# Optimization experiments

Hardware: AMD Instinct MI355X
Metric: run time of the kernel (lower is better)

Reference implementation:

```python
import jax, jax.numpy as jnp
import numpy as np

N = 2_000_000   # active voxels
CIN = 16
COUT = 32
K2 = 9          # 3x3 kernel offsets


def setup_inputs() -> dict:
    key = jax.random.key(0)
    ks = jax.random.split(key, 6)
    x = jax.random.normal(ks[0], (N, CIN), dtype=jnp.float32)
    # per-offset neighbor map: nbr_idx[k, i] = input voxel feeding output i at offset k
    nbr_idx = jax.random.randint(ks[1], (K2, N), 0, N, dtype=jnp.int32)
    nbr_mask = jax.random.uniform(ks[2], (K2, N)) < 0.85
    # center offset is always the voxel itself and always valid
    nbr_idx = nbr_idx.at[K2 // 2].set(jnp.arange(N, dtype=jnp.int32))
    nbr_mask = nbr_mask.at[K2 // 2].set(True)
    s1 = 1.0 / np.sqrt(K2 * CIN)
    s2 = 1.0 / np.sqrt(K2 * COUT)
    sp = 1.0 / np.sqrt(CIN)
    W1 = jax.random.uniform(ks[3], (K2, CIN, COUT), jnp.float32, -s1, s1)
    b1 = jnp.zeros((COUT,), jnp.float32)
    W2 = jax.random.uniform(ks[4], (K2, COUT, COUT), jnp.float32, -s2, s2)
    b2 = jnp.zeros((COUT,), jnp.float32)
    Wp = jax.random.uniform(ks[5], (CIN, COUT), jnp.float32, -sp, sp)
    bp = jnp.zeros((COUT,), jnp.float32)
    return {"x": x, "W1": W1, "b1": b1, "W2": W2, "b2": b2,
            "Wp": Wp, "bp": bp, "nbr_idx": nbr_idx, "nbr_mask": nbr_mask}


def _sparse_conv(feats, W, b, nbr_idx, nbr_mask):
    """Gather-GEMM-accumulate sparse conv.
    feats: [N, Cin]; W: [K2, Cin, Cout]; nbr_idx/nbr_mask: [K2, N].
    Scans over the K2 kernel offsets so only one [N, Cin] gather lives at a time.
    """
    acc0 = jnp.zeros((feats.shape[0], W.shape[-1]), feats.dtype)

    def step(acc, kin):
        idx, m, Wk = kin
        g = feats[idx] * m[:, None].astype(feats.dtype)  # masked gather [N, Cin]
        return acc + g @ Wk, None

    acc, _ = jax.lax.scan(step, acc0, (nbr_idx, nbr_mask, W))
    return acc + b


def reference(x, W1, b1, W2, b2, Wp, bp, nbr_idx, nbr_mask):
    h = jax.nn.relu(_sparse_conv(x, W1, b1, nbr_idx, nbr_mask))
    h = _sparse_conv(h, W2, b2, nbr_idx, nbr_mask)
    identity = x @ Wp + bp  # 1x1 sparse projection (in_ch != out_ch)
    return jax.nn.relu(h + identity)
```

## Files before the change

### kernel.cpp

```cpp
#include <hip/hip_runtime.h>
#include <stdint.h>

#define CIN  16
#define COUT 32
#define K2   9

typedef __attribute__((ext_vector_type(8)))  short bf16x8;
typedef __attribute__((ext_vector_type(16))) float f32x16;
typedef __attribute__((ext_vector_type(4)))  float f32x4;

__device__ __forceinline__ uint16_t f2bf(float f) {
    union { float f; uint32_t u; } a; a.f = f;
    uint32_t u = a.u;
    uint32_t r = u + 0x7FFFu + ((u >> 16) & 1u);
    return (uint16_t)(r >> 16);
}
__device__ __forceinline__ float bf2f(uint32_t b16) {
    union { uint32_t u; float f; } a; a.u = b16 << 16; return a.f;
}

__global__ void detect_mask_kernel(const uint32_t* __restrict__ mw,
                                   int* __restrict__ flag,
                                   float* __restrict__ zrow, int n) {
    int t = threadIdx.x;
    uint32_t w = mw[(size_t)4 * (size_t)n + (size_t)t];
    unsigned long long b = __ballot(w == 1u);
    if (t == 0) *flag = (b == ~0ull) ? 1 : 0;
    if (t < 16) zrow[t] = 0.0f;
}

__global__ void __launch_bounds__(256, 4)
conv1_kernel(const float* __restrict__ x,
             const float* __restrict__ W1,
             const float* __restrict__ b1,
             const int*   __restrict__ nidx,
             const void*  __restrict__ nmask,
             const int*   __restrict__ mflag,
             const char*  __restrict__ zrow,
             uint16_t*    __restrict__ hbuf,
             int n)
{
    __shared__ __align__(16) uint16_t smw[K2 * 2 * 32 * 8];

    for (int i = threadIdx.x; i < K2 * 2 * 32 * 8; i += 256) {
        const int e = i & 7, c2 = (i >> 3) & 31, hf = (i >> 8) & 1, k = i >> 9;
        smw[i] = f2bf(W1[k * (CIN * COUT) + (hf * 8 + e) * COUT + c2]);
    }
    __syncthreads();

    const int lane = threadIdx.x & 63;
    const int wid  = threadIdx.x >> 6;
    const int col  = lane & 31;
    const int half = lane >> 5;
    const int mode32 = *mflag;
    const int*     m32 = (const int*)nmask;
    const uint8_t* m8  = (const uint8_t*)nmask;

    const float bias = b1[col];
    const int ntiles = (n + 31) >> 5;

    for (int tile = blockIdx.x * 4 + wid; tile < ntiles; tile += gridDim.x * 4) {
        const int vbase = tile << 5;
        const int vr = vbase + col;
        const int vc = (vr < n) ? vr : (n - 1);

        int idv[K2];
        uint32_t mb = 0;
        #pragma unroll
        for (int k = 0; k < K2; ++k) {
            const size_t e = (size_t)k * (size_t)n + (size_t)vc;
            idv[k] = __builtin_nontemporal_load(nidx + e);
            const int m = mode32 ? (__builtin_nontemporal_load(m32 + e) != 0)
                                 : (__builtin_nontemporal_load(m8  + e) != 0);
            mb |= (uint32_t)m << k;
        }

        f32x4 ga[K2], gb[K2];
        #pragma unroll
        for (int k = 0; k < K2; ++k) {
            const float* p = ((mb >> k) & 1u)
                ? (x + (size_t)(uint32_t)idv[k] * CIN + half * 8)
                : (const float*)(zrow + half * 32);
            ga[k] = ((const f32x4*)p)[0];
            gb[k] = ((const f32x4*)p)[1];
        }

        f32x16 acc = {};
        #pragma unroll
        for (int k = 0; k < K2; ++k) {
            const bf16x8 Bf = *(const bf16x8*)&smw[((k * 2 + half) * 32 + col) * 8];
            bf16x8 hi, lo;
            #pragma unroll
            for (int e = 0; e < 8; ++e) {
                const float xv = (e < 4) ? ga[k][e] : gb[k][e - 4];
                const uint16_t hb = f2bf(xv);
                hi[e] = (short)hb;
                lo[e] = (short)f2bf(xv - bf2f(hb));
            }
            acc = __builtin_amdgcn_mfma_f32_32x32x16_bf16(hi, Bf, acc, 0, 0, 0);
            acc = __builtin_amdgcn_mfma_f32_32x32x16_bf16(lo, Bf, acc, 0, 0, 0);
        }

        #pragma unroll
        for (int r = 0; r < 16; ++r) {
            const int row = (r & 3) + 8 * (r >> 2) + 4 * half;
            const int vo = vbase + row;
            if (vo < n) {
                const float o = fmaxf(acc[r] + bias, 0.0f);
                hbuf[(size_t)vo * COUT + col] = f2bf(o);
            }
        }
    }
}

__global__ void __launch_bounds__(256, 4)
conv2_kernel(const float* __restrict__ x,
             const float* __restrict__ W2,
             const float* __restrict__ b2,
             const float* __restrict__ Wp,
             const float* __restrict__ bp,
             const int*   __restrict__ nidx,
             const void*  __restrict__ nmask,
             const int*   __restrict__ mflag,
             const char*  __restrict__ zrow,
             const uint16_t* __restrict__ hbuf,
             float*       __restrict__ out,
             int n)
{
    __shared__ __align__(16) uint16_t smw[K2 * 4 * 32 * 8 + 2 * 32 * 8];

    for (int i = threadIdx.x; i < K2 * 4 * 32 * 8 + 2 * 32 * 8; i += 256) {
        uint16_t v;
        if (i < K2 * 4 * 32 * 8) {
            const int e = i & 7, c2 = (i >> 3) & 31, hf = (i >> 8) & 1,
                      cb = (i >> 9) & 1, k = i >> 10;
            v = f2bf(W2[k * (COUT * COUT) + (cb * 16 + hf * 8 + e) * COUT + c2]);
        } else {
            const int j = i - K2 * 4 * 32 * 8;
            const int e = j & 7, c2 = (j >> 3) & 31, hf = (j >> 8) & 1;
            v = f2bf(Wp[(hf * 8 + e) * COUT + c2]);
        }
        smw[i] = v;
    }
    __syncthreads();

    const int lane = threadIdx.x & 63;
    const int wid  = threadIdx.x >> 6;
    const int col  = lane & 31;
    const int half = lane >> 5;
    const int mode32 = *mflag;
    const int*     m32 = (const int*)nmask;
    const uint8_t* m8  = (const uint8_t*)nmask;

    const float bias = b2[col] + bp[col];
    const int ntiles = (n + 31) >> 5;

    for (int tile = blockIdx.x * 4 + wid; tile < ntiles; tile += gridDim.x * 4) {
        const int vbase = tile << 5;
        const int vr = vbase + col;
        const int vc = (vr < n) ? vr : (n - 1);

        int idv[K2];
        uint32_t mb = 0;
        #pragma unroll
        for (int k = 0; k < K2; ++k) {
            const size_t e = (size_t)k * (size_t)n + (size_t)vc;
            idv[k] = __builtin_nontemporal_load(nidx + e);
            const int m = mode32 ? (__builtin_nontemporal_load(m32 + e) != 0)
                                 : (__builtin_nontemporal_load(m8  + e) != 0);
            mb |= (uint32_t)m << k;
        }

        const f32x4* xr = (const f32x4*)(x + (size_t)vc * CIN + half * 8);
        const f32x4 xa = __builtin_nontemporal_load(xr);
        const f32x4 xb = __builtin_nontemporal_load(xr + 1);

        bf16x8 A0[K2], A1[K2];
        #pragma unroll
        for (int k = 0; k < K2; ++k) {
            const char* p = ((mb >> k) & 1u)
                ? (const char*)hbuf + (size_t)(uint32_t)idv[k] * (COUT * 2)
                : zrow;
            A0[k] = *(const bf16x8*)(p + half * 16);
            A1[k] = *(const bf16x8*)(p + 32 + half * 16);
        }

        f32x16 acc = {};

        {
            bf16x8 hi, lo;
            #pragma unroll
            for (int e = 0; e < 8; ++e) {
                const float xv = (e < 4) ? xa[e] : xb[e - 4];
                const uint16_t hb = f2bf(xv);
                hi[e] = (short)hb;
                lo[e] = (short)f2bf(xv - bf2f(hb));
            }
            const bf16x8 Bp = *(const bf16x8*)&smw[K2 * 4 * 32 * 8 + (half * 32 + col) * 8];
            acc = __builtin_amdgcn_mfma_f32_32x32x16_bf16(hi, Bp, acc, 0, 0, 0);
            acc = __builtin_amdgcn_mfma_f32_32x32x16_bf16(lo, Bp, acc, 0, 0, 0);
        }

        #pragma unroll
        for (int k = 0; k < K2; ++k) {
            const bf16x8 B0 = *(const bf16x8*)&smw[(((k * 2 + 0) * 2 + half) * 32 + col) * 8];
            const bf16x8 B1 = *(const bf16x8*)&smw[(((k * 2 + 1) * 2 + half) * 32 + col) * 8];
            acc = __builtin_amdgcn_mfma_f32_32x32x16_bf16(A0[k], B0, acc, 0, 0, 0);
            acc = __builtin_amdgcn_mfma_f32_32x32x16_bf16(A1[k], B1, acc, 0, 0, 0);
        }

        #pragma unroll
        for (int r = 0; r < 16; ++r) {
            const int row = (r & 3) + 8 * (r >> 2) + 4 * half;
            const int vo = vbase + row;
            if (vo < n) {
                const float o = fmaxf(acc[r] + bias, 0.0f);
                __builtin_nontemporal_store(o, out + (size_t)vo * COUT + col);
            }
        }
    }
}

extern "C" void kernel_launch(void* const* d_in, const int* in_sizes, int n_in,
                              void* d_out, int out_size, void* d_ws, size_t ws_size,
                              hipStream_t stream) {
    const float* x    = (const float*)d_in[0];
    const float* W1   = (const float*)d_in[1];
    const float* b1   = (const float*)d_in[2];
    const float* W2   = (const float*)d_in[3];
    const float* b2   = (const float*)d_in[4];
    const float* Wp   = (const float*)d_in[5];
    const float* bp   = (const float*)d_in[6];
    const int*   nidx = (const int*)d_in[7];
    const void*  nmask = d_in[8];
    const int n = in_sizes[0] / CIN;

    int*      mflag = (int*)d_ws;
    float*    zrowf = (float*)((char*)d_ws + 64);
    uint16_t* hbuf  = (uint16_t*)((char*)d_ws + 256);

    detect_mask_kernel<<<1, 64, 0, stream>>>((const uint32_t*)nmask, mflag, zrowf, n);

    const int ntiles = (n + 31) / 32;
    int grid = (ntiles + 3) / 4;
    if (grid > 2048) grid = 2048;

    conv1_kernel<<<grid, 256, 0, stream>>>(x, W1, b1, nidx, nmask, mflag,
                                           (const char*)zrowf, hbuf, n);
    conv2_kernel<<<grid, 256, 0, stream>>>(x, W2, b2, Wp, bp, nidx, nmask, mflag,
                                           (const char*)zrowf, hbuf, (float*)d_out, n);
}
```

Before: 1.007 ms.

## Prefetch next tile's neighbor indices and gather unconditionally, masking after load

Both conv kernels now load the next tile's neighbor indices while the current tile is being processed, taking the index load off the gather's dependency chain. Gathers are always issued from the neighbor index, so they no longer wait on the mask load. The mask is applied after the gather by zeroing the values, which removes the zero-row workspace buffer. Launch bounds change to waves_per_eu(3,4), which allows more registers per thread for the prefetched state. The cost is extra gather traffic for masked neighbors and higher register pressure.

```diff
diff --git a/kernel.cpp b/kernel.cpp
--- a/kernel.cpp
+++ b/kernel.cpp
@@ -20,23 +20,21 @@
 }
 
 __global__ void detect_mask_kernel(const uint32_t* __restrict__ mw,
-                                   int* __restrict__ flag,
-                                   float* __restrict__ zrow, int n) {
+                                   int* __restrict__ flag, int n) {
     int t = threadIdx.x;
     uint32_t w = mw[(size_t)4 * (size_t)n + (size_t)t];
     unsigned long long b = __ballot(w == 1u);
     if (t == 0) *flag = (b == ~0ull) ? 1 : 0;
-    if (t < 16) zrow[t] = 0.0f;
-}
-
-__global__ void __launch_bounds__(256, 4)
+}
+
+__attribute__((amdgpu_waves_per_eu(3, 4)))
+__global__ void __launch_bounds__(256)
 conv1_kernel(const float* __restrict__ x,
              const float* __restrict__ W1,
              const float* __restrict__ b1,
              const int*   __restrict__ nidx,
              const void*  __restrict__ nmask,
              const int*   __restrict__ mflag,
-             const char*  __restrict__ zrow,
              uint16_t*    __restrict__ hbuf,
              int n)
 {
@@ -55,44 +53,60 @@
     const int mode32 = *mflag;
     const int*     m32 = (const int*)nmask;
     const uint8_t* m8  = (const uint8_t*)nmask;
-
     const float bias = b1[col];
+
     const int ntiles = (n + 31) >> 5;
-
-    for (int tile = blockIdx.x * 4 + wid; tile < ntiles; tile += gridDim.x * 4) {
-        const int vbase = tile << 5;
-        const int vr = vbase + col;
-        const int vc = (vr < n) ? vr : (n - 1);
-
-        int idv[K2];
-        uint32_t mb = 0;
-        #pragma unroll
-        for (int k = 0; k < K2; ++k) {
-            const size_t e = (size_t)k * (size_t)n + (size_t)vc;
-            idv[k] = __builtin_nontemporal_load(nidx + e);
-            const int m = mode32 ? (__builtin_nontemporal_load(m32 + e) != 0)
-                                 : (__builtin_nontemporal_load(m8  + e) != 0);
-            mb |= (uint32_t)m << k;
-        }
+    const int stride = gridDim.x * 4;
+    int p = blockIdx.x * 4 + wid;
+    if (p >= ntiles) return;
+
+    int ci[K2];
+    {
+        const int vc = min((p << 5) + col, n - 1);
+        #pragma unroll
+        for (int k = 0; k < K2; ++k)
+            ci[k] = __builtin_nontemporal_load(nidx + (size_t)k * n + vc);
+    }
+
+    for (;;) {
+        const int vbase = p << 5;
+        const int vc = min(vbase + col, n - 1);
 
         f32x4 ga[K2], gb[K2];
         #pragma unroll
         for (int k = 0; k < K2; ++k) {
-            const float* p = ((mb >> k) & 1u)
-                ? (x + (size_t)(uint32_t)idv[k] * CIN + half * 8)
-                : (const float*)(zrow + half * 32);
-            ga[k] = ((const f32x4*)p)[0];
-            gb[k] = ((const f32x4*)p)[1];
+            const f32x4* pg = (const f32x4*)(x + (size_t)(uint32_t)ci[k] * CIN + half * 8);
+            ga[k] = pg[0];
+            gb[k] = pg[1];
+        }
+
+        int mk[K2];
+        #pragma unroll
+        for (int k = 0; k < K2; ++k) {
+            const size_t e = (size_t)k * n + (size_t)vc;
+            mk[k] = mode32 ? __builtin_nontemporal_load(m32 + e)
+                           : (int)__builtin_nontemporal_load(m8 + e);
+        }
+
+        const int pn = p + stride;
+        {
+            const int pc = (pn < ntiles) ? pn : p;
+            const int wc = min((pc << 5) + col, n - 1);
+            #pragma unroll
+            for (int k = 0; k < K2; ++k)
+                ci[k] = __builtin_nontemporal_load(nidx + (size_t)k * n + wc);
         }
 
         f32x16 acc = {};
         #pragma unroll
         for (int k = 0; k < K2; ++k) {
             const bf16x8 Bf = *(const bf16x8*)&smw[((k * 2 + half) * 32 + col) * 8];
+            const bool m = mk[k] != 0;
             bf16x8 hi, lo;
             #pragma unroll
             for (int e = 0; e < 8; ++e) {
-                const float xv = (e < 4) ? ga[k][e] : gb[k][e - 4];
+                float xv = (e < 4) ? ga[k][e] : gb[k][e - 4];
+                xv = m ? xv : 0.0f;
                 const uint16_t hb = f2bf(xv);
                 hi[e] = (short)hb;
                 lo[e] = (short)f2bf(xv - bf2f(hb));
@@ -105,15 +119,17 @@
         for (int r = 0; r < 16; ++r) {
             const int row = (r & 3) + 8 * (r >> 2) + 4 * half;
             const int vo = vbase + row;
-            if (vo < n) {
-                const float o = fmaxf(acc[r] + bias, 0.0f);
-                hbuf[(size_t)vo * COUT + col] = f2bf(o);
-            }
-        }
-    }
-}
-
-__global__ void __launch_bounds__(256, 4)
+            if (vo < n)
+                hbuf[(size_t)vo * COUT + col] = f2bf(fmaxf(acc[r] + bias, 0.0f));
+        }
+
+        if (pn >= ntiles) break;
+        p = pn;
+    }
+}
+
+__attribute__((amdgpu_waves_per_eu(3, 4)))
+__global__ void __launch_bounds__(256)
 conv2_kernel(const float* __restrict__ x,
              const float* __restrict__ W2,
              const float* __restrict__ b2,
@@ -122,7 +138,6 @@
              const int*   __restrict__ nidx,
              const void*  __restrict__ nmask,
              const int*   __restrict__ mflag,
-             const char*  __restrict__ zrow,
              const uint16_t* __restrict__ hbuf,
              float*       __restrict__ out,
              int n)
@@ -151,25 +166,24 @@
     const int mode32 = *mflag;
     const int*     m32 = (const int*)nmask;
     const uint8_t* m8  = (const uint8_t*)nmask;
-
     const float bias = b2[col] + bp[col];
+
     const int ntiles = (n + 31) >> 5;
-
-    for (int tile = blockIdx.x * 4 + wid; tile < ntiles; tile += gridDim.x * 4) {
-        const int vbase = tile << 5;
-        const int vr = vbase + col;
-        const int vc = (vr < n) ? vr : (n - 1);
-
-        int idv[K2];
-        uint32_t mb = 0;
-        #pragma unroll
-        for (int k = 0; k < K2; ++k) {
-            const size_t e = (size_t)k * (size_t)n + (size_t)vc;
-            idv[k] = __builtin_nontemporal_load(nidx + e);
-            const int m = mode32 ? (__builtin_nontemporal_load(m32 + e) != 0)
-                                 : (__builtin_nontemporal_load(m8  + e) != 0);
-            mb |= (uint32_t)m << k;
-        }
+    const int stride = gridDim.x * 4;
+    int p = blockIdx.x * 4 + wid;
+    if (p >= ntiles) return;
+
+    int ci[K2];
+    {
+        const int vc = min((p << 5) + col, n - 1);
+        #pragma unroll
+        for (int k = 0; k < K2; ++k)
+            ci[k] = __builtin_nontemporal_load(nidx + (size_t)k * n + vc);
+    }
+
+    for (;;) {
+        const int vbase = p << 5;
+        const int vc = min(vbase + col, n - 1);
 
         const f32x4* xr = (const f32x4*)(x + (size_t)vc * CIN + half * 8);
         const f32x4 xa = __builtin_nontemporal_load(xr);
@@ -178,16 +192,32 @@
         bf16x8 A0[K2], A1[K2];
         #pragma unroll
         for (int k = 0; k < K2; ++k) {
-            const char* p = ((mb >> k) & 1u)
-                ? (const char*)hbuf + (size_t)(uint32_t)idv[k] * (COUT * 2)
-                : zrow;
-            A0[k] = *(const bf16x8*)(p + half * 16);
-            A1[k] = *(const bf16x8*)(p + 32 + half * 16);
+            const char* pg = (const char*)hbuf + (size_t)(uint32_t)ci[k] * (COUT * 2);
+            A0[k] = *(const bf16x8*)(pg + half * 16);
+            A1[k] = *(const bf16x8*)(pg + 32 + half * 16);
+        }
+
+        int mk[K2];
+        #pragma unroll
+        for (int k = 0; k < K2; ++k) {
+            const size_t e = (size_t)k * n + (size_t)vc;
+            mk[k] = mode32 ? __builtin_nontemporal_load(m32 + e)
+                           : (int)__builtin_nontemporal_load(m8 + e);
+        }
+
+        const int pn = p + stride;
+        {
+            const int pc = (pn < ntiles) ? pn : p;
+            const int wc = min((pc << 5) + col, n - 1);
+            #pragma unroll
+            for (int k = 0; k < K2; ++k)
+                ci[k] = __builtin_nontemporal_load(nidx + (size_t)k * n + wc);
         }
 
         f32x16 acc = {};
 
         {
+            const bf16x8 Bp = *(const bf16x8*)&smw[K2 * 4 * 32 * 8 + (half * 32 + col) * 8];
             bf16x8 hi, lo;
             #pragma unroll
             for (int e = 0; e < 8; ++e) {
@@ -196,7 +226,6 @@
                 hi[e] = (short)hb;
                 lo[e] = (short)f2bf(xv - bf2f(hb));
             }
-            const bf16x8 Bp = *(const bf16x8*)&smw[K2 * 4 * 32 * 8 + (half * 32 + col) * 8];
             acc = __builtin_amdgcn_mfma_f32_32x32x16_bf16(hi, Bp, acc, 0, 0, 0);
             acc = __builtin_amdgcn_mfma_f32_32x32x16_bf16(lo, Bp, acc, 0, 0, 0);
         }
@@ -205,19 +234,25 @@
         for (int k = 0; k < K2; ++k) {
             const bf16x8 B0 = *(const bf16x8*)&smw[(((k * 2 + 0) * 2 + half) * 32 + col) * 8];
             const bf16x8 B1 = *(const bf16x8*)&smw[(((k * 2 + 1) * 2 + half) * 32 + col) * 8];
-            acc = __builtin_amdgcn_mfma_f32_32x32x16_bf16(A0[k], B0, acc, 0, 0, 0);
-            acc = __builtin_amdgcn_mfma_f32_32x32x16_bf16(A1[k], B1, acc, 0, 0, 0);
+            const bf16x8 zf = {};
+            const bool m = mk[k] != 0;
+            const bf16x8 a0 = m ? A0[k] : zf;
+            const bf16x8 a1 = m ? A1[k] : zf;
+            acc = __builtin_amdgcn_mfma_f32_32x32x16_bf16(a0, B0, acc, 0, 0, 0);
+            acc = __builtin_amdgcn_mfma_f32_32x32x16_bf16(a1, B1, acc, 0, 0, 0);
         }
 
         #pragma unroll
         for (int r = 0; r < 16; ++r) {
             const int row = (r & 3) + 8 * (r >> 2) + 4 * half;
             const int vo = vbase + row;
-            if (vo < n) {
-                const float o = fmaxf(acc[r] + bias, 0.0f);
-                __builtin_nontemporal_store(o, out + (size_t)vo * COUT + col);
-            }
-        }
+            if (vo < n)
+                __builtin_nontemporal_store(fmaxf(acc[r] + bias, 0.0f),
+                                            out + (size_t)vo * COUT + col);
+        }
+
+        if (pn >= ntiles) break;
+        p = pn;
     }
 }
 
@@ -236,17 +271,15 @@
     const int n = in_sizes[0] / CIN;
 
     int*      mflag = (int*)d_ws;
-    float*    zrowf = (float*)((char*)d_ws + 64);
     uint16_t* hbuf  = (uint16_t*)((char*)d_ws + 256);
 
-    detect_mask_kernel<<<1, 64, 0, stream>>>((const uint32_t*)nmask, mflag, zrowf, n);
+    detect_mask_kernel<<<1, 64, 0, stream>>>((const uint32_t*)nmask, mflag, n);
 
     const int ntiles = (n + 31) / 32;
     int grid = (ntiles + 3) / 4;
     if (grid > 2048) grid = 2048;
 
-    conv1_kernel<<<grid, 256, 0, stream>>>(x, W1, b1, nidx, nmask, mflag,
-                                           (const char*)zrowf, hbuf, n);
+    conv1_kernel<<<grid, 256, 0, stream>>>(x, W1, b1, nidx, nmask, mflag, hbuf, n);
     conv2_kernel<<<grid, 256, 0, stream>>>(x, W2, b2, Wp, bp, nidx, nmask, mflag,
-                                           (const char*)zrowf, hbuf, (float*)d_out, n);
-}
+                                           hbuf, (float*)d_out, n);
+}
```

Result: slower. 1.115 ms (+10.7%).
